# Performance work log

Measured on AMD Instinct MI355X. Metric: run time of the kernel, lower is better.

Reference implementation:

```python
import jax, jax.numpy as jnp
import numpy as np

# static config (must match init_kwargs)
B, HIS, N, DIN = 16, 13, 400, 16
HID, S, PRED, LAYERS = 256, 4, 12, 3
NG = S * N  # nodes in the combined virtual graph
DEG = 8     # avg out-degree of base adjacency
EPS = 1e-5


def _build_graph():
    """Reproduce _combine_graph (offset bug included) + edge weights."""
    rng = np.random.default_rng(0)
    cols = np.argsort(rng.random((N, N)), axis=1)[:, :DEG]  # [N, DEG] distinct cols per row
    w = rng.uniform(0.1, 1.0, size=(N, DEG)).astype(np.float32)
    rows = np.repeat(np.arange(N), DEG)
    c = cols.ravel()
    off = (S - 1) * N
    # first block rows: [adj | adj]; last diagonal block: adj
    src = np.concatenate([rows, rows, rows + off]).astype(np.int32)
    dst = np.concatenate([c, c + N, c + off]).astype(np.int32)
    ew = np.concatenate([w.ravel(), w.ravel(), w.ravel()]).astype(np.float32)
    return src, dst, ew


def _checkpoints():
    mark, chp = S, []
    while mark < HIS:
        chp.append(mark)
        mark += S - 1
    if chp[-1] != HIS:
        chp.append(HIS)
    return chp


def setup_inputs() -> dict:
    key = jax.random.key(0)
    ks = jax.random.split(key, 9)
    src, dst, ew = _build_graph()
    sc = 0.05
    return {
        "inputs": jax.random.normal(ks[0], (B, HIS, N, DIN), jnp.float32),
        "W_in": jax.random.normal(ks[1], (DIN, HID), jnp.float32) * sc,
        "b_in": jax.random.normal(ks[2], (HID,), jnp.float32) * sc,
        "gcn_W": jax.random.normal(ks[3], (LAYERS, HID, HID), jnp.float32) * sc,
        "gcn_b": jax.random.normal(ks[4], (LAYERS, HID), jnp.float32) * sc,
        "W1": jax.random.normal(ks[5], (1, PRED), jnp.float32) * sc,
        "b1": jax.random.normal(ks[6], (PRED,), jnp.float32) * sc,
        "W2": jax.random.normal(ks[7], (HID, 1), jnp.float32) * sc,
        "b2": jax.random.normal(ks[8], (1,), jnp.float32) * sc,
        "edge_w": jnp.asarray(ew),
        "src": jnp.asarray(src),
        "dst": jnp.asarray(dst),
    }


def _gcn(h, src, dst, edge_w, inv_out, inv_in, gcn_W, gcn_b):
    """LAYERS-deep GraphConv (norm='both', edge weights), ReLU between layers.
    h: [B, NG, HID]. Dropout is identity (eval)."""
    seg = jax.vmap(lambda m: jax.ops.segment_sum(m, dst, num_segments=NG))
    for i in range(LAYERS):
        hs = h * inv_out[None, :, None]          # D_out^{-1/2} on src side
        msg = hs[:, src, :] * edge_w[None, :, None]  # [B, E, HID]
        agg = seg(msg) * inv_in[None, :, None]   # D_in^{-1/2} on dst side
        h_new = agg @ gcn_W[i] + gcn_b[i]
        h = jax.nn.relu(h_new) if i < LAYERS - 1 else h_new
    return h


def reference(inputs, W_in, b_in, gcn_W, gcn_b, W1, b1, W2, b2, edge_w, src, dst):
    # unweighted degrees for symmetric normalization (guard isolated nodes)
    ones = jnp.ones_like(edge_w)
    out_deg = jnp.zeros((NG,), jnp.float32).at[src].add(ones)
    in_deg = jnp.zeros((NG,), jnp.float32).at[dst].add(ones)
    inv_out = jax.lax.rsqrt(jnp.maximum(out_deg, 1.0))
    inv_in = jax.lax.rsqrt(jnp.maximum(in_deg, 1.0))

    x = inputs @ W_in + b_in  # [B, HIS, N, HID]
    last = None
    left = 0
    for idx, right in enumerate(_checkpoints()):
        if idx == 0:
            fs = x[:, left:right]                       # [B, S, N, HID]
        else:
            fs = jnp.concatenate([last, x[:, left:right]], axis=1)
        h = fs.reshape(B, NG, HID)
        res = h
        h = _gcn(h, src, dst, edge_w, inv_out, inv_in, gcn_W, gcn_b) + res
        # nn.LayerNorm([B*S*N, HID], elementwise_affine=False) on a tensor of
        # exactly that shape => normalize over ALL elements jointly
        h = (h - h.mean()) * jax.lax.rsqrt(h.var() + EPS)
        h = h.reshape(B, S, N, HID)
        last = h[:, -1:, :, :]  # [B, 1, N, HID]
        left = right

    t = jnp.transpose(last, (0, 3, 2, 1))   # [B, HID, N, 1]
    o = t @ W1 + b1                          # [B, HID, N, PRED]
    o = jnp.transpose(o, (0, 3, 2, 1))       # [B, PRED, N, HID]
    o = jax.nn.relu(o)
    return o @ W2 + b2                       # [B, PRED, N, 1]
```

## Files before the change

### kernel.cpp

```cpp
#include <hip/hip_runtime.h>

#define BB 16
#define HIS 13
#define NN 400
#define DIN 16
#define HID 256
#define PRED 12
#define NE 9600
#define EPSF 1e-5f
#define HSZ ((size_t)25600*256)
#define BAND ((size_t)NN*BB*HID)
#define ROWS_BAND (NN*BB)
#define CSR_CAP 6144

typedef __attribute__((ext_vector_type(8))) short short8v;
typedef __attribute__((ext_vector_type(4))) float f32x4;

__device__ __forceinline__ short f2bf(float x) {
    unsigned u = __float_as_uint(x);
    return (short)((u + 0x7FFF + ((u >> 16) & 1)) >> 16);
}
__device__ __forceinline__ float bf2f(short x) {
    return __uint_as_float(((unsigned)(unsigned short)x) << 16);
}
__device__ __forceinline__ void gload16(const void* g, void* l) {
    __builtin_amdgcn_global_load_lds((const __attribute__((address_space(1))) void*)g,
                                     (__attribute__((address_space(3))) void*)l,
                                     16, 0, 0);
}

__global__ __launch_bounds__(256) void k_prep(
    const int* __restrict__ src, const int* __restrict__ dst,
    const float* __restrict__ ew, const float* __restrict__ gcn_W,
    const float* __restrict__ inp, const float* __restrict__ W_in,
    const float* __restrict__ b_in, const float* __restrict__ gb2,
    float* __restrict__ inv_in, float* __restrict__ csum,
    int* __restrict__ csr_off, int* __restrict__ csr_src,
    float* __restrict__ cf1, float* __restrict__ cf2,
    short* __restrict__ Wt, short* __restrict__ xproj,
    float* __restrict__ stats)
{
    __shared__ __align__(16) char SM[17408];
    int t = threadIdx.x, bi = blockIdx.x;
    if (bi == 0) {
        int* odeg = (int*)SM;
        int* ideg = odeg + 1600;
        int* cnt  = ideg + 400;
        int* offl = cnt + 400;
        int* scan_t = offl + 401;
        float* csuml = (float*)(scan_t + 256);
        for (int g = t; g < 1600; g += 256) odeg[g] = 0;
        for (int g = t; g < 400; g += 256) { ideg[g] = 0; cnt[g] = 0; csuml[g] = 0.f; }
        if (t == 9) stats[9] = (1.0f - EPSF) * (float)HSZ;
        __syncthreads();
        for (int e = t; e < NE; e += 256) atomicAdd(&odeg[src[e]], 1);
        for (int e = t; e < 3200; e += 256) atomicAdd(&ideg[dst[e]], 1);
        __syncthreads();
        int s = 0, p0 = 0, p1 = 0;
        if (t < 200) {
            p0 = (ideg[2 * t] + 7) & ~7;
            p1 = (ideg[2 * t + 1] + 7) & ~7;
            s = p0 + p1;
        }
        scan_t[t] = s;
        __syncthreads();
        for (int o = 1; o < 256; o <<= 1) {
            int v = (t >= o) ? scan_t[t - o] : 0;
            __syncthreads();
            scan_t[t] += v;
            __syncthreads();
        }
        if (t < 200) { int base = scan_t[t] - s; offl[2 * t] = base; offl[2 * t + 1] = base + p0; }
        if (t == 255) offl[400] = scan_t[255];
        __syncthreads();
        int cap = offl[400];
        for (int g = t; g < 401; g += 256) csr_off[g] = offl[g];
        for (int g = t; g < 400; g += 256) inv_in[g] = rsqrtf(fmaxf((float)ideg[g], 1.f));
        for (int i = t; i < cap; i += 256) { csr_src[i] = 0; cf1[i] = 0.f; cf2[i] = 0.f; }
        __syncthreads();
        for (int e = t; e < 3200; e += 256) {
            int d = dst[e];
            int r = src[e];
            int p = offl[d] + atomicAdd(&cnt[d], 1);
            float w = ew[e];
            float c1 = w * rsqrtf(fmaxf((float)odeg[r], 1.f));
            float c2 = w * rsqrtf(fmaxf((float)odeg[1200 + r], 1.f));
            csr_src[p] = r;
            cf1[p] = c1;
            cf2[p] = c2;
            atomicAdd(&csuml[d], c1);
        }
        __syncthreads();
        for (int g = t; g < 400; g += 256) csum[g] = csuml[g];
    } else if (bi <= 48) {
        float (*S)[65] = (float(*)[65])SM;
        int tile = bi - 1;
        int l = tile / 16, sub = tile % 16;
        int k0 = (sub >> 2) * 64, n0 = (sub & 3) * 64;
        int tr = t >> 6, tc = t & 63;
#pragma unroll
        for (int i = 0; i < 16; ++i) {
            int r = i * 4 + tr;
            S[r][tc] = gcn_W[(size_t)l * 65536 + (size_t)(k0 + r) * 256 + n0 + tc];
        }
        __syncthreads();
#pragma unroll
        for (int i = 0; i < 16; ++i) {
            int n = i * 4 + tr;
            Wt[(size_t)l * 65536 + (size_t)(n0 + n) * 256 + k0 + tc] = f2bf(S[tc][n]);
        }
    } else {
        float* rbuf = (float*)SM;
        float wr[16];
#pragma unroll
        for (int d = 0; d < 16; ++d) wr[d] = W_in[d * 256 + t];
        float bvv = b_in[t];
        int job0 = (bi - 49) * 4;
        int time = job0 / 400;
        int n0 = job0 % 400;
        bool isStat = (time == 2 || time == 5 || time == 8 || time == 11);
        float gb = isStat ? gb2[t] : 0.f;
        float s1 = 0.f, s2 = 0.f;
        for (int j = 0; j < 4; ++j) {
            int n = n0 + j;
            float acc[16];
#pragma unroll
            for (int b = 0; b < 16; ++b) acc[b] = bvv;
#pragma unroll
            for (int b = 0; b < 16; ++b) {
                const float* xr = inp + (((size_t)b * HIS + time) * NN + n) * DIN;
#pragma unroll
                for (int d = 0; d < 16; ++d) acc[b] = fmaf(xr[d], wr[d], acc[b]);
            }
            if (isStat) {
#pragma unroll
                for (int b = 0; b < 16; ++b) {
                    float v = acc[b] + gb;
                    s1 += v; s2 += v * v;
                }
            } else {
                size_t gbase = (size_t)time * BAND + ((size_t)n * 16) * 256 + t;
#pragma unroll
                for (int b = 0; b < 16; ++b) xproj[gbase + (size_t)b * 256] = f2bf(acc[b]);
            }
        }
        if (isStat) {
#pragma unroll
            for (int o = 32; o > 0; o >>= 1) {
                s1 += __shfl_down(s1, o, 64);
                s2 += __shfl_down(s2, o, 64);
            }
            int wid = t >> 6, lane = t & 63;
            if (lane == 0) { rbuf[wid] = s1; rbuf[4 + wid] = s2; }
            __syncthreads();
            if (t == 0) {
                int it = (time - 2) / 3;
                atomicAdd(&stats[it * 2],     rbuf[0] + rbuf[1] + rbuf[2] + rbuf[3]);
                atomicAdd(&stats[it * 2 + 1], rbuf[4] + rbuf[5] + rbuf[6] + rbuf[7]);
            }
        }
    }
}

template <int MODE>
__global__ __launch_bounds__(256) void k_layer(
    const short* __restrict__ hX, const short* __restrict__ hY,
    const float* __restrict__ stA, const float* __restrict__ csum,
    const float* __restrict__ inv_in, const int* __restrict__ csr_off,
    const int* __restrict__ csr_src, const float* __restrict__ cf1,
    const float* __restrict__ cf2,
    const short* __restrict__ Bt, const float* __restrict__ bias,
    const short* __restrict__ resX0, const float* __restrict__ stR,
    const short* __restrict__ resX1, const short* __restrict__ resY,
    short* __restrict__ C, float* __restrict__ stats)
{
    __shared__ short As[32][264];
    __shared__ short Bs[2][8192];
    __shared__ float red[512];
    int tid = threadIdx.x;
    int wid = tid >> 6, l = tid & 63;
    int l15 = l & 15, l4 = l >> 4;
    int blk = blockIdx.x;
    int isY = blk >= 200;
    int gl = (isY ? blk - 200 : blk) * 2;
    int rowL0 = gl * 16;
    int wn = wid * 64;
    const short* hsrc = isY ? hY : hX;
    const float* cf = isY ? cf2 : cf1;

    float am = 1.f, moff = 0.f;
    if (MODE == 0 && !isY) {
        float mean = stA[0] * (1.f / (float)HSZ);
        float var  = stA[1] * (1.f / (float)HSZ) - mean * mean;
        float istd = rsqrtf(var + EPSF);
        am = istd; moff = mean * istd;
    }

    int br = l >> 2;
    int kd = (l & 3) ^ ((br >> 1) & 3);
    for (int ch = wid; ch < 16; ch += 4)
        gload16(Bt + ((size_t)(ch * 16 + br)) * 256 + kd * 8, &Bs[0][ch * 512]);

    {
        int b = tid >> 4, hsc = (tid & 15) * 16;
        const size_t lane_off = (size_t)b * HID + hsc;
        for (int gi = 0; gi < 2; ++gi) {
            int g = gl + gi;
            int beg = csr_off[g], end = csr_off[g + 1];
            float acc[16];
#pragma unroll
            for (int i = 0; i < 16; ++i) acc[i] = 0.f;
            for (int j = beg; j < end; j += 8) {
                int ss[8]; float cc[8];
#pragma unroll
                for (int u = 0; u < 8; ++u) { ss[u] = csr_src[j + u]; cc[u] = cf[j + u]; }
                short8v va[8], vb[8];
#pragma unroll
                for (int u = 0; u < 8; ++u) {
                    const short8v* q = (const short8v*)&hsrc[(size_t)ss[u] * 4096 + lane_off];
                    va[u] = q[0]; vb[u] = q[1];
                }
#pragma unroll
                for (int u = 0; u < 8; ++u) {
#pragma unroll
                    for (int i = 0; i < 8; ++i) {
                        acc[i]     = fmaf(cc[u], bf2f(va[u][i]), acc[i]);
                        acc[8 + i] = fmaf(cc[u], bf2f(vb[u][i]), acc[8 + i]);
                    }
                }
            }
            float s = inv_in[g];
            float addv = (MODE == 0 && !isY) ? (-moff * csum[g]) : 0.f;
            short8v o0, o1;
#pragma unroll
            for (int i = 0; i < 8; ++i) o0[i] = f2bf(s * fmaf(am, acc[i], addv));
#pragma unroll
            for (int i = 0; i < 8; ++i) o1[i] = f2bf(s * fmaf(am, acc[8 + i], addv));
            int row = gi * 16 + b;
            *(short8v*)&As[row][hsc]     = o0;
            *(short8v*)&As[row][hsc + 8] = o1;
        }
    }
    __syncthreads();

    f32x4 cacc[2][4] = {};
    int xsw = (l4 ^ ((l15 >> 1) & 3)) * 8;
    for (int kc = 0; kc < 8; ++kc) {
        int cur = kc & 1;
        if (kc < 7) {
            int k0n = (kc + 1) * 32;
            for (int ch = wid; ch < 16; ch += 4)
                gload16(Bt + ((size_t)(ch * 16 + br)) * 256 + k0n + kd * 8,
                        &Bs[cur ^ 1][ch * 512]);
        }
        int k0 = kc * 32;
        short8v av[2], bv[4];
#pragma unroll
        for (int mi = 0; mi < 2; ++mi)
            av[mi] = *(const short8v*)&As[mi * 16 + l15][k0 + l4 * 8];
#pragma unroll
        for (int ni = 0; ni < 4; ++ni)
            bv[ni] = *(const short8v*)&Bs[cur][(wn + ni * 16 + l15) * 32 + xsw];
#pragma unroll
        for (int mi = 0; mi < 2; ++mi)
#pragma unroll
            for (int ni = 0; ni < 4; ++ni)
                cacc[mi][ni] = __builtin_amdgcn_mfma_f32_16x16x32_bf16(
                    av[mi], bv[ni], cacc[mi][ni], 0, 0, 0);
        __syncthreads();
    }

    if (MODE <= 1) {
#pragma unroll
        for (int ni = 0; ni < 4; ++ni) {
            int col = wn + ni * 16 + l15;
            float bvv = bias[col];
#pragma unroll
            for (int mi = 0; mi < 2; ++mi) {
#pragma unroll
                for (int r = 0; r < 4; ++r) {
                    float v = fmaxf(cacc[mi][ni][r] + bvv, 0.f);
                    As[mi * 16 + l4 * 4 + r][col] = f2bf(v);
                }
            }
        }
        __syncthreads();
        int row = tid >> 3, cs = (tid & 7) * 32;
        size_t gb = ((size_t)(isY ? ROWS_BAND : 0) + rowL0 + row) * HID + cs;
#pragma unroll
        for (int i = 0; i < 4; ++i)
            *(short8v*)&C[gb + i * 8] = *(const short8v*)&As[row][cs + i * 8];
    } else {
        float s1 = 0.f, s2 = 0.f;
        if (!isY) {
            float meanR = stR[0] * (1.f / (float)HSZ);
            float varR  = stR[1] * (1.f / (float)HSZ) - meanR * meanR;
            float istdR = rsqrtf(varR + EPSF);
#pragma unroll
            for (int ni = 0; ni < 4; ++ni) {
                int col = wn + ni * 16 + l15;
                float bvv = bias[col];
#pragma unroll
                for (int mi = 0; mi < 2; ++mi) {
#pragma unroll
                    for (int r = 0; r < 4; ++r) {
                        int rowg = rowL0 + mi * 16 + l4 * 4 + r;
                        size_t ix = (size_t)rowg * HID + col;
                        float base = cacc[mi][ni][r] + bvv;
                        float v1 = base + (bf2f(resX0[ix]) - meanR) * istdR;
                        float v2 = base + bf2f(resX1[ix]);
                        s1 += v1 + v2;
                        s2 += v1 * v1 + v2 * v2;
                    }
                }
            }
        } else {
#pragma unroll
            for (int ni = 0; ni < 4; ++ni) {
                int col = wn + ni * 16 + l15;
                float bvv = bias[col];
#pragma unroll
                for (int mi = 0; mi < 2; ++mi) {
#pragma unroll
                    for (int r = 0; r < 4; ++r) {
                        int rowl = mi * 16 + l4 * 4 + r;
                        size_t ix = (size_t)(rowL0 + rowl) * HID + col;
                        float v = cacc[mi][ni][r] + bvv + bf2f(resY[ix]);
                        s1 += v; s2 += v * v;
                        As[rowl][col] = f2bf(v);
                    }
                }
            }
            __syncthreads();
            int row = tid >> 3, cs = (tid & 7) * 32;
            size_t gb = (size_t)(rowL0 + row) * HID + cs;
#pragma unroll
            for (int i = 0; i < 4; ++i)
                *(short8v*)&C[gb + i * 8] = *(const short8v*)&As[row][cs + i * 8];
        }
        red[tid] = s1; red[256 + tid] = s2;
        __syncthreads();
        for (int o = 128; o > 0; o >>= 1) {
            if (tid < o) { red[tid] += red[tid + o]; red[256 + tid] += red[256 + tid + o]; }
            __syncthreads();
        }
        if (tid == 0) { atomicAdd(&stats[0], red[0]); atomicAdd(&stats[1], red[256]); }
    }
}

__global__ void k_head(const short* __restrict__ hlast, const float* __restrict__ st,
                       const float* __restrict__ W1, const float* __restrict__ b1,
                       const float* __restrict__ W2, const float* __restrict__ b2,
                       float* __restrict__ out) {
    float mean = st[0] * (1.0f / (float)HSZ);
    float var  = st[1] * (1.0f / (float)HSZ) - mean * mean;
    float istd = rsqrtf(var + EPSF);
    int n = blockIdx.x, b = blockIdx.y, tid = threadIdx.x;
    float v  = (bf2f(hlast[((size_t)n * BB + b) * HID + tid]) - mean) * istd;
    float w2 = W2[tid];
    float b2v = b2[0];
    __shared__ float ps[4];
    for (int p = 0; p < PRED; ++p) {
        float t = fmaxf(fmaf(v, W1[p], b1[p]), 0.f) * w2;
#pragma unroll
        for (int o = 32; o > 0; o >>= 1) t += __shfl_down(t, o, 64);
        int wid = tid >> 6, lane = tid & 63;
        if (lane == 0) ps[wid] = t;
        __syncthreads();
        if (tid == 0) out[(size_t)(b * PRED + p) * NN + n] = ps[0] + ps[1] + ps[2] + ps[3] + b2v;
        __syncthreads();
    }
}

extern "C" void kernel_launch(void* const* d_in, const int* in_sizes, int n_in,
                              void* d_out, int out_size, void* d_ws, size_t ws_size,
                              hipStream_t stream) {
    const float* inp   = (const float*)d_in[0];
    const float* W_in  = (const float*)d_in[1];
    const float* b_in  = (const float*)d_in[2];
    const float* gcn_W = (const float*)d_in[3];
    const float* gcn_b = (const float*)d_in[4];
    const float* W1    = (const float*)d_in[5];
    const float* b1    = (const float*)d_in[6];
    const float* W2    = (const float*)d_in[7];
    const float* b2    = (const float*)d_in[8];
    const float* ew    = (const float*)d_in[9];
    const int*   src   = (const int*)d_in[10];
    const int*   dst   = (const int*)d_in[11];
    float* out = (float*)d_out;

    char* w = (char*)d_ws;
    auto alloc = [&](size_t bytes) {
        char* p = w;
        w += (bytes + 255) & ~(size_t)255;
        return p;
    };
    short* hA    = (short*)alloc((size_t)2 * ROWS_BAND * HID * 2);
    short* hB    = (short*)alloc((size_t)2 * ROWS_BAND * HID * 2);
    short* hl0   = (short*)alloc(BAND * 2);
    short* hl1   = (short*)alloc(BAND * 2);
    short* xproj = (short*)alloc((size_t)13 * BAND * 2);
    short* Wt    = (short*)alloc((size_t)3 * 65536 * 2);
    float* inv_in  = (float*)alloc(400 * 4);
    float* csum    = (float*)alloc(400 * 4);
    int*   csr_off = (int*)alloc(401 * 4);
    int*   csr_srcv= (int*)alloc(CSR_CAP * 4);
    float* cf1     = (float*)alloc(CSR_CAP * 4);
    float* cf2     = (float*)alloc(CSR_CAP * 4);
    float* stats   = (float*)alloc(12 * 4);

    hipMemsetAsync(stats, 0, 12 * 4, stream);
    k_prep<<<1349, 256, 0, stream>>>(src, dst, ew, gcn_W, inp, W_in, b_in,
                                     gcn_b + 512, inv_in, csum, csr_off,
                                     csr_srcv, cf1, cf2, Wt, xproj, stats);

    short* hlbuf[2] = {hl0, hl1};
    const int lefts[4] = {0, 4, 7, 10};
    const size_t RB = (size_t)ROWS_BAND * HID;
    for (int it = 0; it < 4; ++it) {
        int t1 = (it == 0) ? 1 : lefts[it];
        int t3 = (it == 0) ? 3 : lefts[it] + 2;
        const short* hlp = (it == 0) ? xproj : hlbuf[(it - 1) & 1];
        const float* stA = (it == 0) ? stats + 8 : stats + (it - 1) * 2;
        short* cur = hlbuf[it & 1];
        k_layer<0><<<400, 256, 0, stream>>>(hlp, xproj + (size_t)t3 * BAND, stA, csum,
                                            inv_in, csr_off, csr_srcv, cf1, cf2,
                                            Wt, gcn_b,
                                            nullptr, nullptr, nullptr, nullptr,
                                            hA, nullptr);
        k_layer<1><<<400, 256, 0, stream>>>(hA, hA + RB, stats + 8, csum,
                                            inv_in, csr_off, csr_srcv, cf1, cf2,
                                            Wt + 65536, gcn_b + 256,
                                            nullptr, nullptr, nullptr, nullptr,
                                            hB, nullptr);
        k_layer<2><<<400, 256, 0, stream>>>(hB, hB + RB, stats + 8, csum,
                                            inv_in, csr_off, csr_srcv, cf1, cf2,
                                            Wt + 131072, gcn_b + 512,
                                            hlp, stA, xproj + (size_t)t1 * BAND,
                                            xproj + (size_t)t3 * BAND,
                                            cur, stats + it * 2);
    }

    k_head<<<dim3(NN, BB), 256, 0, stream>>>(hlbuf[1], stats + 6, W1, b1, W2, b2, out);
}
```

Before: 287.9 us.

## Hoist independent Y-band GCN work for all iterations into one batched launch

The GCN work for the Y band (rows fed only from input projections) does not depend on earlier iterations, so all four iterations' Y-band blocks now run together in the first three launches (1000 blocks each). Later iterations only launch the dependent X-band blocks (200 each). This removes serial dependence and gives small launches more parallel work, at the cost of extra workspace buffers per iteration and underfilled later launches.

Result: no change. 292.8 us (+1.7%).

```diff
diff --git a/kernel.cpp b/kernel.cpp
--- a/kernel.cpp
+++ b/kernel.cpp
@@ -162,17 +162,17 @@
     }
 }
 
-template <int MODE>
-__global__ __launch_bounds__(256) void k_layer(
-    const short* __restrict__ hX, const short* __restrict__ hY,
-    const float* __restrict__ stA, const float* __restrict__ csum,
-    const float* __restrict__ inv_in, const int* __restrict__ csr_off,
-    const int* __restrict__ csr_src, const float* __restrict__ cf1,
-    const float* __restrict__ cf2,
-    const short* __restrict__ Bt, const float* __restrict__ bias,
-    const short* __restrict__ resX0, const float* __restrict__ stR,
-    const short* __restrict__ resX1, const short* __restrict__ resY,
-    short* __restrict__ C, float* __restrict__ stats)
+template <int P>
+__global__ __launch_bounds__(256) void k_pipe(
+    const short* __restrict__ xproj,
+    short* __restrict__ hAX, short* __restrict__ hBX,
+    short* __restrict__ hAY, short* __restrict__ hBY,
+    short* __restrict__ hl4,
+    const short* __restrict__ Wt, const float* __restrict__ gcn_b,
+    const float* __restrict__ csum, const float* __restrict__ inv_in,
+    const int* __restrict__ csr_off, const int* __restrict__ csr_src,
+    const float* __restrict__ cf1, const float* __restrict__ cf2,
+    float* __restrict__ stats, int xit, int nx)
 {
     __shared__ short As[32][264];
     __shared__ short Bs[2][8192];
@@ -181,19 +181,46 @@
     int wid = tid >> 6, l = tid & 63;
     int l15 = l & 15, l4 = l >> 4;
     int blk = blockIdx.x;
-    int isY = blk >= 200;
-    int gl = (isY ? blk - 200 : blk) * 2;
+    bool isX = blk < nx;
+    int gl, statIdx = 0;
+    const short *hsrc, *resA = nullptr, *resB = nullptr;
+    short* Cout = nullptr;
+    const float* cf;
+    const float* stA = nullptr;
+
+    if (isX) {
+        gl = blk * 2;
+        cf = cf1;
+        const short* hlp = (xit == 0) ? xproj : hl4 + (size_t)(xit - 1) * BAND;
+        stA = (xit == 0) ? stats + 8 : stats + (xit - 1) * 2;
+        if (P == 0)      { hsrc = hlp; Cout = hAX; }
+        else if (P == 1) { hsrc = hAX; Cout = hBX; }
+        else             { hsrc = hBX; resA = hlp;
+                           resB = xproj + (size_t)(1 + 3 * xit) * BAND;
+                           statIdx = xit * 2; }
+    } else {
+        int yb = blk - nx;
+        int yit = yb / 200;
+        gl = (yb % 200) * 2;
+        cf = cf2;
+        const short* xb3 = xproj + (size_t)(3 + 3 * yit) * BAND;
+        if (P == 0)      { hsrc = xb3; Cout = hAY + (size_t)yit * BAND; }
+        else if (P == 1) { hsrc = hAY + (size_t)yit * BAND; Cout = hBY + (size_t)yit * BAND; }
+        else             { hsrc = hBY + (size_t)yit * BAND; Cout = hl4 + (size_t)yit * BAND;
+                           resA = xb3; statIdx = yit * 2; }
+    }
+    const float* bias = gcn_b + P * 256;
+    const short* Bt = Wt + P * 65536;
     int rowL0 = gl * 16;
     int wn = wid * 64;
-    const short* hsrc = isY ? hY : hX;
-    const float* cf = isY ? cf2 : cf1;
-
-    float am = 1.f, moff = 0.f;
-    if (MODE == 0 && !isY) {
+
+    float am = 1.f, moff = 0.f, meanR = 0.f, istdR = 1.f;
+    if (isX && (P == 0 || P == 2)) {
         float mean = stA[0] * (1.f / (float)HSZ);
         float var  = stA[1] * (1.f / (float)HSZ) - mean * mean;
         float istd = rsqrtf(var + EPSF);
-        am = istd; moff = mean * istd;
+        if (P == 0) { am = istd; moff = mean * istd; }
+        else        { meanR = mean; istdR = istd; }
     }
 
     int br = l >> 2;
@@ -230,7 +257,7 @@
                 }
             }
             float s = inv_in[g];
-            float addv = (MODE == 0 && !isY) ? (-moff * csum[g]) : 0.f;
+            float addv = (P == 0 && isX) ? (-moff * csum[g]) : 0.f;
             short8v o0, o1;
 #pragma unroll
             for (int i = 0; i < 8; ++i) o0[i] = f2bf(s * fmaf(am, acc[i], addv));
@@ -270,7 +297,7 @@
         __syncthreads();
     }
 
-    if (MODE <= 1) {
+    if (P <= 1) {
 #pragma unroll
         for (int ni = 0; ni < 4; ++ni) {
             int col = wn + ni * 16 + l15;
@@ -286,16 +313,13 @@
         }
         __syncthreads();
         int row = tid >> 3, cs = (tid & 7) * 32;
-        size_t gb = ((size_t)(isY ? ROWS_BAND : 0) + rowL0 + row) * HID + cs;
+        size_t gb = (size_t)(rowL0 + row) * HID + cs;
 #pragma unroll
         for (int i = 0; i < 4; ++i)
-            *(short8v*)&C[gb + i * 8] = *(const short8v*)&As[row][cs + i * 8];
+            *(short8v*)&Cout[gb + i * 8] = *(const short8v*)&As[row][cs + i * 8];
     } else {
         float s1 = 0.f, s2 = 0.f;
-        if (!isY) {
-            float meanR = stR[0] * (1.f / (float)HSZ);
-            float varR  = stR[1] * (1.f / (float)HSZ) - meanR * meanR;
-            float istdR = rsqrtf(varR + EPSF);
+        if (isX) {
 #pragma unroll
             for (int ni = 0; ni < 4; ++ni) {
                 int col = wn + ni * 16 + l15;
@@ -307,8 +331,8 @@
                         int rowg = rowL0 + mi * 16 + l4 * 4 + r;
                         size_t ix = (size_t)rowg * HID + col;
                         float base = cacc[mi][ni][r] + bvv;
-                        float v1 = base + (bf2f(resX0[ix]) - meanR) * istdR;
-                        float v2 = base + bf2f(resX1[ix]);
+                        float v1 = base + (bf2f(resA[ix]) - meanR) * istdR;
+                        float v2 = base + bf2f(resB[ix]);
                         s1 += v1 + v2;
                         s2 += v1 * v1 + v2 * v2;
                     }
@@ -325,7 +349,7 @@
                     for (int r = 0; r < 4; ++r) {
                         int rowl = mi * 16 + l4 * 4 + r;
                         size_t ix = (size_t)(rowL0 + rowl) * HID + col;
-                        float v = cacc[mi][ni][r] + bvv + bf2f(resY[ix]);
+                        float v = cacc[mi][ni][r] + bvv + bf2f(resA[ix]);
                         s1 += v; s2 += v * v;
                         As[rowl][col] = f2bf(v);
                     }
@@ -336,7 +360,7 @@
             size_t gb = (size_t)(rowL0 + row) * HID + cs;
 #pragma unroll
             for (int i = 0; i < 4; ++i)
-                *(short8v*)&C[gb + i * 8] = *(const short8v*)&As[row][cs + i * 8];
+                *(short8v*)&Cout[gb + i * 8] = *(const short8v*)&As[row][cs + i * 8];
         }
         red[tid] = s1; red[256 + tid] = s2;
         __syncthreads();
@@ -344,7 +368,10 @@
             if (tid < o) { red[tid] += red[tid + o]; red[256 + tid] += red[256 + tid + o]; }
             __syncthreads();
         }
-        if (tid == 0) { atomicAdd(&stats[0], red[0]); atomicAdd(&stats[1], red[256]); }
+        if (tid == 0) {
+            atomicAdd(&stats[statIdx],     red[0]);
+            atomicAdd(&stats[statIdx + 1], red[256]);
+        }
     }
 }
 
@@ -395,11 +422,12 @@
         w += (bytes + 255) & ~(size_t)255;
         return p;
     };
-    short* hA    = (short*)alloc((size_t)2 * ROWS_BAND * HID * 2);
-    short* hB    = (short*)alloc((size_t)2 * ROWS_BAND * HID * 2);
-    short* hl0   = (short*)alloc(BAND * 2);
-    short* hl1   = (short*)alloc(BAND * 2);
     short* xproj = (short*)alloc((size_t)13 * BAND * 2);
+    short* hAX   = (short*)alloc(BAND * 2);
+    short* hBX   = (short*)alloc(BAND * 2);
+    short* hAY   = (short*)alloc((size_t)4 * BAND * 2);
+    short* hBY   = (short*)alloc((size_t)4 * BAND * 2);
+    short* hl4   = (short*)alloc((size_t)4 * BAND * 2);
     short* Wt    = (short*)alloc((size_t)3 * 65536 * 2);
     float* inv_in  = (float*)alloc(400 * 4);
     float* csum    = (float*)alloc(400 * 4);
@@ -414,32 +442,27 @@
                                      gcn_b + 512, inv_in, csum, csr_off,
                                      csr_srcv, cf1, cf2, Wt, xproj, stats);
 
-    short* hlbuf[2] = {hl0, hl1};
-    const int lefts[4] = {0, 4, 7, 10};
-    const size_t RB = (size_t)ROWS_BAND * HID;
-    for (int it = 0; it < 4; ++it) {
-        int t1 = (it == 0) ? 1 : lefts[it];
-        int t3 = (it == 0) ? 3 : lefts[it] + 2;
-        const short* hlp = (it == 0) ? xproj : hlbuf[(it - 1) & 1];
-        const float* stA = (it == 0) ? stats + 8 : stats + (it - 1) * 2;
-        short* cur = hlbuf[it & 1];
-        k_layer<0><<<400, 256, 0, stream>>>(hlp, xproj + (size_t)t3 * BAND, stA, csum,
-                                            inv_in, csr_off, csr_srcv, cf1, cf2,
-                                            Wt, gcn_b,
-                                            nullptr, nullptr, nullptr, nullptr,
-                                            hA, nullptr);
-        k_layer<1><<<400, 256, 0, stream>>>(hA, hA + RB, stats + 8, csum,
-                                            inv_in, csr_off, csr_srcv, cf1, cf2,
-                                            Wt + 65536, gcn_b + 256,
-                                            nullptr, nullptr, nullptr, nullptr,
-                                            hB, nullptr);
-        k_layer<2><<<400, 256, 0, stream>>>(hB, hB + RB, stats + 8, csum,
-                                            inv_in, csr_off, csr_srcv, cf1, cf2,
-                                            Wt + 131072, gcn_b + 512,
-                                            hlp, stA, xproj + (size_t)t1 * BAND,
-                                            xproj + (size_t)t3 * BAND,
-                                            cur, stats + it * 2);
-    }
-
-    k_head<<<dim3(NN, BB), 256, 0, stream>>>(hlbuf[1], stats + 6, W1, b1, W2, b2, out);
-}
+    k_pipe<0><<<1000, 256, 0, stream>>>(xproj, hAX, hBX, hAY, hBY, hl4, Wt, gcn_b,
+                                        csum, inv_in, csr_off, csr_srcv, cf1, cf2,
+                                        stats, 0, 200);
+    k_pipe<1><<<1000, 256, 0, stream>>>(xproj, hAX, hBX, hAY, hBY, hl4, Wt, gcn_b,
+                                        csum, inv_in, csr_off, csr_srcv, cf1, cf2,
+                                        stats, 0, 200);
+    k_pipe<2><<<1000, 256, 0, stream>>>(xproj, hAX, hBX, hAY, hBY, hl4, Wt, gcn_b,
+                                        csum, inv_in, csr_off, csr_srcv, cf1, cf2,
+                                        stats, 0, 200);
+    for (int xit = 1; xit < 4; ++xit) {
+        k_pipe<0><<<200, 256, 0, stream>>>(xproj, hAX, hBX, hAY, hBY, hl4, Wt, gcn_b,
+                                           csum, inv_in, csr_off, csr_srcv, cf1, cf2,
+                                           stats, xit, 200);
+        k_pipe<1><<<200, 256, 0, stream>>>(xproj, hAX, hBX, hAY, hBY, hl4, Wt, gcn_b,
+                                           csum, inv_in, csr_off, csr_srcv, cf1, cf2,
+                                           stats, xit, 200);
+        k_pipe<2><<<200, 256, 0, stream>>>(xproj, hAX, hBX, hAY, hBY, hl4, Wt, gcn_b,
+                                           csum, inv_in, csr_off, csr_srcv, cf1, cf2,
+                                           stats, xit, 200);
+    }
+
+    k_head<<<dim3(NN, BB), 256, 0, stream>>>(hl4 + (size_t)3 * BAND, stats + 6,
+                                             W1, b1, W2, b2, out);
+}
```
